# Performance work log

Hardware: AMD Instinct MI355X
Metric: run time of the kernel (lower is better)

## Reference

```python
import jax, jax.numpy as jnp
import numpy as np

NB_STEPS = 50
ALPHA = 0.9
NUM_RNN_STEPS = 2
B = 4096
NUM_FEATURE = 100
IN_D = 5
HIDDEN = [64, 64, 64]
P1 = (1.1, 1.1, 1.5, 2.0, 2.5)   # IntegrandNN_outer_level powers
P2 = (1.5, 2.0, 2.5, 3.0, 3.5)   # IntegrandNN powers


def _cc(nb_steps):
    # Clenshaw-Curtis weights/steps, identical to UMNN's compute_cc_weights
    n = nb_steps
    i = np.arange(n + 1, dtype=np.float64).reshape(-1, 1)
    lam = np.cos(i @ i.T * np.pi / n)
    lam[:, 0] = 0.5
    lam[:, -1] *= 0.5
    lam = lam * 2.0 / n
    W = np.zeros(n + 1)
    even = np.arange(0, n + 1, 2)
    W[even] = 2.0 / (1.0 - even.astype(np.float64) ** 2)
    W[0] = 1.0
    ccw = (lam.T @ W).astype(np.float32)                         # [n+1]
    steps = np.cos(np.arange(n + 1) * np.pi / n).astype(np.float32)  # [n+1]
    return jnp.asarray(ccw), jnp.asarray(steps)

CC_W, CC_S = _cc(NB_STEPS)


def _mlp(xh, Ws, bs):
    # Linear+ReLU stack with ELU on the last layer (ReLU popped, ELU appended)
    h = xh
    for W, b in zip(Ws[:-1], bs[:-1]):
        h = jax.nn.relu(h @ W.T + b)
    return jax.nn.elu(h @ Ws[-1].T + bs[-1])


def _integrand(x, h, Ws, bs, Wf, powers):
    z = _mlp(jnp.concatenate([x, h], axis=1), Ws, bs) + 1.0      # [N,1], z >= 0
    feats = jnp.concatenate([z ** p for p in powers], axis=1)    # [N,5]
    return jax.nn.relu((1.0 / (feats + 1.0)) @ Wf.T)             # [N,1]


def _integrate(x0, xT, h, f):
    # ParallelNeuralIntegral forward: CC quadrature of f from x0 to xT
    Bn, S = x0.shape[0], NB_STEPS + 1
    X = x0[:, None, :] + (xT - x0)[:, None, :] * (CC_S[None, :, None] + 1.0) / 2.0  # [B,S,1]
    hs = jnp.broadcast_to(h[:, None, :], (Bn, S, h.shape[1])).reshape(-1, h.shape[1])
    dz = f(X.reshape(-1, 1), hs).reshape(Bn, S, 1)
    return (dz * CC_W[None, :, None]).sum(1) * (xT - x0) / 2.0   # [B,1]


def setup_inputs() -> dict:
    key = jax.random.key(0)
    ks = jax.random.split(key, 24)
    def lin(k, o, i):
        return jax.random.normal(k, (o, i), jnp.float32) / np.sqrt(i)
    d = {}
    d["x_"] = jax.random.normal(ks[0], (B, NUM_FEATURE), jnp.float32)
    d["h_"] = jax.random.normal(ks[1], (B, IN_D - 1), jnp.float32)
    d["log_weight"] = jnp.ones((1, NUM_FEATURE), jnp.float32)     # reset_parameters -> 1
    d["sigmoid_param"] = jnp.zeros((1,), jnp.float32)
    sizes = [IN_D] + HIDDEN + [1]
    for tag, base in (("f1", 2), ("f2", 12)):
        for li, (i, o) in enumerate(zip(sizes[:-1], sizes[1:])):
            d[f"{tag}_W{li}"] = lin(ks[base + 2 * li], o, i)
            d[f"{tag}_b{li}"] = jnp.zeros((o,), jnp.float32)
        d[f"{tag}_Wf"] = jnp.abs(lin(ks[base + 9], 1, 5))         # reset_params -> abs
    return d


def reference(x_, h_, log_weight, sigmoid_param,
              f1_W0, f1_b0, f1_W1, f1_b1, f1_W2, f1_b2, f1_W3, f1_b3, f1_Wf,
              f2_W0, f2_b0, f2_W1, f2_b1, f2_W2, f2_b2, f2_W3, f2_b3, f2_Wf):
    f1Ws = [f1_W0, f1_W1, f1_W2, f1_W3]; f1bs = [f1_b0, f1_b1, f1_b2, f1_b3]
    f2Ws = [f2_W0, f2_W1, f2_W2, f2_W3]; f2bs = [f2_b0, f2_b1, f2_b2, f2_b3]
    f1 = lambda x, h: _integrand(x, h, f1Ws, f1bs, f1_Wf, P1)
    f2 = lambda x, h: _integrand(x, h, f2Ws, f2bs, f2_Wf, P2)

    # modular function: linear to [B,1] then sum over dim 1 -> [B,1]
    xm = jnp.sum(x_ * log_weight[0], axis=1, keepdims=True)
    lam = jax.nn.sigmoid(sigmoid_param[0])

    I1 = jnp.zeros_like(xm)
    I2 = jnp.zeros_like(xm)
    out_first = None
    for _ in range(NUM_RNN_STEPS):
        x = (1.0 - lam) * xm + lam * I1
        x2 = (1.0 - lam) * xm + lam * I2
        out_first = f1(x2, h_)
        I1 = _integrate(jnp.zeros_like(x), x, h_, f1)
        xmax = jnp.max(x2) + 10.0
        xfinal = jnp.zeros_like(x) + xmax
        I2 = (1.0 / ALPHA) * _integrate(x2, xfinal, h_, f2)
    return I1, out_first, I2
```

## Files before the change

### kernel.cpp

```cpp
#include <hip/hip_runtime.h>
#include <math.h>

typedef _Float16 half8v __attribute__((ext_vector_type(8)));
typedef _Float16 half4v __attribute__((ext_vector_type(4)));
typedef _Float16 half2v __attribute__((ext_vector_type(2)));
typedef float float4v __attribute__((ext_vector_type(4)));

#define BB    4096
#define INV_ALPHA (1.0f/0.9f)

#define WS_CCW  0
#define WS_CCS  64
#define WS_LAM  128
#define WS_PM16 160
#define WS_PM   256
#define WS_XM   512
#define WS_X    (WS_XM + BB)
#define WS_X2   (WS_X + BB)
#define WS_H    16384
#define H_NET   8192
#define H_W2    4096
#define H_W0    16384
#define H_W3    20480

#if defined(__has_builtin)
#if __has_builtin(__builtin_amdgcn_rcpf)
#define FRCP(x) __builtin_amdgcn_rcpf(x)
#endif
#if __has_builtin(__builtin_amdgcn_exp2f)
#define FEXP2(x) __builtin_amdgcn_exp2f(x)
#endif
#if __has_builtin(__builtin_amdgcn_logf)
#define FLOG2(x) __builtin_amdgcn_logf(x)
#endif
#endif
#ifndef FRCP
#define FRCP(x) (1.0f / (x))
#endif
#ifndef FEXP2
#define FEXP2(x) exp2f(x)
#endif
#ifndef FLOG2
#define FLOG2(x) log2f(x)
#endif

__device__ __forceinline__ int swz(int row, int cb) {
    return (row << 6) + (((cb ^ (row & 7)) & 7) << 3);
}

__device__ __forceinline__ half4v pk_relu4(float4v c) {
#if defined(__has_builtin) && __has_builtin(__builtin_amdgcn_cvt_pkrtz)
    half2v a = __builtin_bit_cast(half2v,
        __builtin_amdgcn_cvt_pkrtz(fmaxf(c[0], 0.0f), fmaxf(c[1], 0.0f)));
    half2v b = __builtin_bit_cast(half2v,
        __builtin_amdgcn_cvt_pkrtz(fmaxf(c[2], 0.0f), fmaxf(c[3], 0.0f)));
    half4v o; o[0] = a[0]; o[1] = a[1]; o[2] = b[0]; o[3] = b[1];
    return o;
#else
    half4v o;
    o[0] = (_Float16)fmaxf(c[0], 0.0f); o[1] = (_Float16)fmaxf(c[1], 0.0f);
    o[2] = (_Float16)fmaxf(c[2], 0.0f); o[3] = (_Float16)fmaxf(c[3], 0.0f);
    return o;
#endif
}

__global__ void k_setup(const float* __restrict__ x_, const float* __restrict__ lw,
                        const float* __restrict__ sp,
                        const float* __restrict__ f1W0, const float* __restrict__ f1W1,
                        const float* __restrict__ f1W2, const float* __restrict__ f1W3,
                        const float* __restrict__ f2W0, const float* __restrict__ f2W1,
                        const float* __restrict__ f2W2, const float* __restrict__ f2W3,
                        float* __restrict__ ws, float* __restrict__ out) {
    _Float16* wh = (_Float16*)(ws + WS_H);
    const int blk = blockIdx.x, tid = threadIdx.x;
    if (blk < 256) {
        int wave = tid >> 6, lane = tid & 63;
        float vmax = -1e30f;
        for (int r = 0; r < 4; ++r) {
            int row = blk * 16 + wave * 4 + r;
            float v = 0.0f;
            for (int i = lane; i < 100; i += 64) v = fmaf(x_[row * 100 + i], lw[i], v);
            #pragma unroll
            for (int off = 32; off > 0; off >>= 1) v += __shfl_xor(v, off, 64);
            if (lane == 0) ws[WS_XM + row] = v;
            vmax = fmaxf(vmax, v);
        }
        __shared__ float sm[4];
        if (lane == 0) sm[wave] = vmax;
        __syncthreads();
        if (tid == 0)
            ws[WS_PM + blk] = fmaxf(fmaxf(sm[0], sm[1]), fmaxf(sm[2], sm[3]));
    } else if (blk < 272) {
        int t = (blk - 256) * 256 + tid;
        wh[t]                = (_Float16)f1W1[t];
        wh[H_W2 + t]         = (_Float16)f1W2[t];
        wh[H_NET + t]        = (_Float16)f2W1[t];
        wh[H_NET + H_W2 + t] = (_Float16)f2W2[t];
        if (t < 2048) {
            int j = t >> 5, k = t & 31;
            wh[H_W0 + t]        = (k < 5) ? (_Float16)f1W0[j * 5 + k] : (_Float16)0.0f;
            wh[H_W0 + 2048 + t] = (k < 5) ? (_Float16)f2W0[j * 5 + k] : (_Float16)0.0f;
        }
        if (t < 64) {
            wh[H_W3 + t]      = (_Float16)f1W3[t];
            wh[H_W3 + 64 + t] = (_Float16)f2W3[t];
        }
    } else if (blk == 272) {
        if (tid == 64) ws[WS_LAM] = 1.0f / (1.0f + expf(-sp[0]));
        if (tid <= 50) {
            int s = tid;
            ws[WS_CCS + s] = cospif((float)s / 50.0f);
            float acc = 0.0f;
            for (int a = 0; a <= 50; ++a) {
                float w;
                if (a == 0) w = 1.0f;
                else if ((a & 1) == 0) w = 2.0f / (1.0f - (float)(a * a));
                else continue;
                float l;
                if (s == 0) l = 0.5f;
                else {
                    int m = (a * s) % 100;
                    l = cospif((float)m / 50.0f);
                    if (s == 50) l *= 0.5f;
                }
                acc += l * 0.04f * w;
            }
            ws[WS_CCW + s] = acc;
        }
    } else {
        int t = (blk - 273) * 256 + tid;
        out[t < BB ? t : BB + t] = 0.0f;
    }
}

__global__ void k_pre(float* __restrict__ ws, float* __restrict__ out) {
    int b = blockIdx.x * 256 + threadIdx.x;
    float lam = ws[WS_LAM];
    float m = ws[WS_XM + b];
    float xv  = (1.0f - lam) * m + lam * out[b];
    float x2v = (1.0f - lam) * m + lam * out[2 * BB + b];
    ws[WS_X + b] = xv;
    ws[WS_X2 + b] = x2v;
    out[b] = 0.0f;
    out[2 * BB + b] = 0.0f;
    __shared__ float red[256];
    red[threadIdx.x] = x2v;
    __syncthreads();
    #pragma unroll
    for (int off = 128; off > 0; off >>= 1) {
        if (threadIdx.x < off)
            red[threadIdx.x] = fmaxf(red[threadIdx.x], red[threadIdx.x + off]);
        __syncthreads();
    }
    if (threadIdx.x == 0) ws[WS_PM16 + blockIdx.x] = red[0];
}

__global__ __launch_bounds__(64, 2) void k_int(
    int mode, float* __restrict__ ws, const float* __restrict__ h_,
    const float* __restrict__ f1b0, const float* __restrict__ f1b1,
    const float* __restrict__ f1b2, const float* __restrict__ f1b3,
    const float* __restrict__ f1Wf,
    const float* __restrict__ f2b0, const float* __restrict__ f2b1,
    const float* __restrict__ f2b2, const float* __restrict__ f2b3,
    const float* __restrict__ f2Wf,
    float* __restrict__ out)
{
    __shared__ _Float16 act[64 * 64];

    const int blk = blockIdx.x;
    const int lane = threadIdx.x;
    const int lo = lane & 15, q = lane >> 4;

    const float* xm = ws + WS_XM;
    const float* xarr = ws + WS_X;
    const float* x2arr = ws + WS_X2;
    const _Float16* wh = (const _Float16*)(ws + WS_H);
    const float lam = ws[WS_LAM];
    const float oml = 1.0f - lam;

    const bool is_of = (blk >= 2048);
    int base, w = 0, np;
    bool u2;
    if (is_of) {
        base = (blk - 2048) << 6; u2 = false; np = 1;
    } else {
        int g = blk >> 4;
        w = blk & 15;
        u2 = (g >= 64);
        base = (g & 63) << 6;
        np = (w < 3) ? 4 : 3;
    }

    const _Float16* W0h = wh + H_W0 + (u2 ? 2048 : 0);
    const _Float16* W1h = wh + (u2 ? H_NET : 0);
    const _Float16* W2h = W1h + H_W2;
    const _Float16* W3h = wh + H_W3 + (u2 ? 64 : 0);
    const float* B0 = u2 ? f2b0 : f1b0;
    const float* B1 = u2 ? f2b1 : f1b1;
    const float* B2 = u2 ? f2b2 : f1b2;
    const float* B3 = u2 ? f2b3 : f1b3;
    const float* WF = u2 ? f2Wf : f1Wf;
    const float p0 = u2 ? 1.5f : 1.1f;
    const float p1 = u2 ? 2.0f : 1.1f;
    const float p2 = u2 ? 2.5f : 1.5f;
    const float p3 = u2 ? 3.0f : 2.0f;
    const float p4 = u2 ? 3.5f : 2.5f;

    half8v A0w[4], A1w[4][2], A2w[4][2];
    float4v b0r[4], b1r[4], b2r[4];
    half4v w3r[4];
    #pragma unroll
    for (int m = 0; m < 4; ++m) {
        A0w[m]    = *(const half8v*)(W0h + (16 * m + lo) * 32 + q * 8);
        A1w[m][0] = *(const half8v*)(W1h + (16 * m + lo) * 64 + q * 8);
        A1w[m][1] = *(const half8v*)(W1h + (16 * m + lo) * 64 + 32 + q * 8);
        A2w[m][0] = *(const half8v*)(W2h + (16 * m + lo) * 64 + q * 8);
        A2w[m][1] = *(const half8v*)(W2h + (16 * m + lo) * 64 + 32 + q * 8);
        b0r[m] = *(const float4v*)(B0 + 16 * m + q * 4);
        b1r[m] = *(const float4v*)(B1 + 16 * m + q * 4);
        b2r[m] = *(const float4v*)(B2 + 16 * m + q * 4);
        w3r[m] = *(const half4v*)(W3h + 16 * m + 4 * q);
    }
    const float B3s = B3[0];
    const float wf0 = WF[0], wf1 = WF[1], wf2 = WF[2], wf3 = WF[3], wf4 = WF[4];

    float xr_r[4];
    float4 h4r[4];
    #pragma unroll
    for (int n = 0; n < 4; ++n) {
        int idx = base + 16 * n + lo;
        float v;
        if (is_of)      v = x2arr[idx];
        else if (mode)  v = u2 ? x2arr[idx] : xarr[idx];
        else            v = oml * xm[idx];
        xr_r[n] = v;
        h4r[n] = ((const float4*)h_)[idx];
    }

    float xmax = 0.0f;
    if (u2) {
        if (mode) {
            float v = (lane < 16) ? ws[WS_PM16 + lane] : -1e30f;
            #pragma unroll
            for (int off = 32; off > 0; off >>= 1) v = fmaxf(v, __shfl_xor(v, off, 64));
            xmax = v + 10.0f;
        } else {
            const float* pm = ws + WS_PM;
            float v = fmaxf(fmaxf(pm[lane], pm[lane + 64]),
                            fmaxf(pm[lane + 128], pm[lane + 192]));
            #pragma unroll
            for (int off = 32; off > 0; off >>= 1) v = fmaxf(v, __shfl_xor(v, off, 64));
            xmax = oml * v + 10.0f;
        }
    }

    float acc = 0.0f;

    #pragma clang loop unroll(disable)
    for (int p = 0; p < np; ++p) {
        const int s = w + 16 * p;
        float t = 0.0f, ccw_s = 0.0f;
        if (!is_of) {
            t = (ws[WS_CCS + s] + 1.0f) * 0.5f;
            ccw_s = ws[WS_CCW + s];
        }

        half8v Bf0[4];
        #pragma unroll
        for (int n = 0; n < 4; ++n) {
            float xin;
            if (is_of)   xin = xr_r[n];
            else if (u2) xin = fmaf(t, xmax - xr_r[n], xr_r[n]);
            else         xin = xr_r[n] * t;
            half8v e;
            e[0] = (_Float16)xin; e[1] = (_Float16)h4r[n].x; e[2] = (_Float16)h4r[n].y;
            e[3] = (_Float16)h4r[n].z; e[4] = (_Float16)h4r[n].w;
            e[5] = (_Float16)0.0f; e[6] = (_Float16)0.0f; e[7] = (_Float16)0.0f;
            half8v z;
            #pragma unroll
            for (int t2 = 0; t2 < 8; ++t2) z[t2] = (_Float16)0.0f;
            Bf0[n] = (q == 0) ? e : z;
        }

        #pragma unroll
        for (int m = 0; m < 4; ++m)
            #pragma unroll
            for (int n = 0; n < 4; ++n) {
                float4v c = __builtin_amdgcn_mfma_f32_16x16x32_f16(A0w[m], Bf0[n], b0r[m], 0, 0, 0);
                *(half4v*)(act + swz(16 * n + lo, 2 * m + (q >> 1)) + 4 * (q & 1)) = pk_relu4(c);
            }

        {
            half8v Bf[2][4];
            #pragma unroll
            for (int kb = 0; kb < 2; ++kb)
                #pragma unroll
                for (int n = 0; n < 4; ++n)
                    Bf[kb][n] = *(const half8v*)(act + swz(16 * n + lo, 4 * kb + q));
            #pragma unroll
            for (int m = 0; m < 4; ++m)
                #pragma unroll
                for (int n = 0; n < 4; ++n) {
                    float4v c = __builtin_amdgcn_mfma_f32_16x16x32_f16(A1w[m][0], Bf[0][n], b1r[m], 0, 0, 0);
                    c = __builtin_amdgcn_mfma_f32_16x16x32_f16(A1w[m][1], Bf[1][n], c, 0, 0, 0);
                    *(half4v*)(act + swz(16 * n + lo, 2 * m + (q >> 1)) + 4 * (q & 1)) = pk_relu4(c);
                }
        }

        float part[4] = {0.0f, 0.0f, 0.0f, 0.0f};
        {
            half8v Bf[2][4];
            #pragma unroll
            for (int kb = 0; kb < 2; ++kb)
                #pragma unroll
                for (int n = 0; n < 4; ++n)
                    Bf[kb][n] = *(const half8v*)(act + swz(16 * n + lo, 4 * kb + q));
            #pragma unroll
            for (int m = 0; m < 4; ++m)
                #pragma unroll
                for (int n = 0; n < 4; ++n) {
                    float4v c = __builtin_amdgcn_mfma_f32_16x16x32_f16(A2w[m][0], Bf[0][n], b2r[m], 0, 0, 0);
                    c = __builtin_amdgcn_mfma_f32_16x16x32_f16(A2w[m][1], Bf[1][n], c, 0, 0, 0);
                    #pragma unroll
                    for (int e = 0; e < 4; ++e)
                        part[n] = fmaf((float)w3r[m][e], fmaxf(c[e], 0.0f), part[n]);
                }
        }

        #pragma unroll
        for (int n = 0; n < 4; ++n) {
            part[n] += __shfl_xor(part[n], 16, 64);
            part[n] += __shfl_xor(part[n], 32, 64);
        }
        float y = B3s + (q == 0 ? part[0] : q == 1 ? part[1] : q == 2 ? part[2] : part[3]);

        if (y <= 0.0f) y = FEXP2(y * 1.44269504f) - 1.0f;
        float z = y + 1.0f;
        float lg = FLOG2(z);
        float g = wf0 * FRCP(FEXP2(p0 * lg) + 1.0f)
                + wf1 * FRCP(FEXP2(p1 * lg) + 1.0f)
                + wf2 * FRCP(FEXP2(p2 * lg) + 1.0f)
                + wf3 * FRCP(FEXP2(p3 * lg) + 1.0f)
                + wf4 * FRCP(FEXP2(p4 * lg) + 1.0f);
        float val = fmaxf(g, 0.0f);

        if (is_of) { out[BB + base + lane] = val; return; }
        acc += ccw_s * val;
    }

    const float x_l = (q == 0 ? xr_r[0] : q == 1 ? xr_r[1] : q == 2 ? xr_r[2] : xr_r[3]);
    if (!u2) {
        atomicAdd(out + base + lane, acc * x_l * 0.5f);
    } else {
        atomicAdd(out + 2 * BB + base + lane, acc * (xmax - x_l) * 0.5f * INV_ALPHA);
    }
}

extern "C" void kernel_launch(void* const* d_in, const int* in_sizes, int n_in,
                              void* d_out, int out_size, void* d_ws, size_t ws_size,
                              hipStream_t stream) {
    const float* x_  = (const float*)d_in[0];
    const float* h_  = (const float*)d_in[1];
    const float* lw  = (const float*)d_in[2];
    const float* sp  = (const float*)d_in[3];
    const float* f1W0 = (const float*)d_in[4];   const float* f1b0 = (const float*)d_in[5];
    const float* f1W1 = (const float*)d_in[6];   const float* f1b1 = (const float*)d_in[7];
    const float* f1W2 = (const float*)d_in[8];   const float* f1b2 = (const float*)d_in[9];
    const float* f1W3 = (const float*)d_in[10];  const float* f1b3 = (const float*)d_in[11];
    const float* f1Wf = (const float*)d_in[12];
    const float* f2W0 = (const float*)d_in[13];  const float* f2b0 = (const float*)d_in[14];
    const float* f2W1 = (const float*)d_in[15];  const float* f2b1 = (const float*)d_in[16];
    const float* f2W2 = (const float*)d_in[17];  const float* f2b2 = (const float*)d_in[18];
    const float* f2W3 = (const float*)d_in[19];  const float* f2b3 = (const float*)d_in[20];
    const float* f2Wf = (const float*)d_in[21];
    float* out = (float*)d_out;
    float* ws  = (float*)d_ws;

    k_setup<<<305, 256, 0, stream>>>(x_, lw, sp,
                                     f1W0, f1W1, f1W2, f1W3,
                                     f2W0, f2W1, f2W2, f2W3, ws, out);
    k_int<<<2048, 64, 0, stream>>>(0, ws, h_,
        f1b0, f1b1, f1b2, f1b3, f1Wf, f2b0, f2b1, f2b2, f2b3, f2Wf, out);
    k_pre<<<16, 256, 0, stream>>>(ws, out);
    k_int<<<2112, 64, 0, stream>>>(1, ws, h_,
        f1b0, f1b1, f1b2, f1b3, f1Wf, f2b0, f2b1, f2b2, f2b3, f2Wf, out);
}
```

Measured before the change: 144.4 us.

## Split quadrature steps across more blocks and load weights per layer

Doubles the k_int grid so each 64-thread block handles 1-2 quadrature steps instead of 3-4, raising parallelism. MLP weight fragments are now loaded from global/L2 inside each layer loop rather than kept in registers for the whole kernel, and launch bounds go to 3 waves per EU to raise occupancy. k_pre switches to 64-thread blocks with a wavefront shuffle reduction, so xmax reads exactly 64 partial maxima. The cost is redundant weight and bias loads per block and more atomics or partial-sum writes.

After: 225.7 us. +56.3%, slower.

```diff
diff --git a/kernel.cpp b/kernel.cpp
--- a/kernel.cpp
+++ b/kernel.cpp
@@ -134,7 +134,7 @@
 }
 
 __global__ void k_pre(float* __restrict__ ws, float* __restrict__ out) {
-    int b = blockIdx.x * 256 + threadIdx.x;
+    int b = blockIdx.x * 64 + threadIdx.x;
     float lam = ws[WS_LAM];
     float m = ws[WS_XM + b];
     float xv  = (1.0f - lam) * m + lam * out[b];
@@ -143,19 +143,13 @@
     ws[WS_X2 + b] = x2v;
     out[b] = 0.0f;
     out[2 * BB + b] = 0.0f;
-    __shared__ float red[256];
-    red[threadIdx.x] = x2v;
-    __syncthreads();
+    float v = x2v;
     #pragma unroll
-    for (int off = 128; off > 0; off >>= 1) {
-        if (threadIdx.x < off)
-            red[threadIdx.x] = fmaxf(red[threadIdx.x], red[threadIdx.x + off]);
-        __syncthreads();
-    }
-    if (threadIdx.x == 0) ws[WS_PM16 + blockIdx.x] = red[0];
-}
-
-__global__ __launch_bounds__(64, 2) void k_int(
+    for (int off = 32; off > 0; off >>= 1) v = fmaxf(v, __shfl_xor(v, off, 64));
+    if (threadIdx.x == 0) ws[WS_PM16 + blockIdx.x] = v;
+}
+
+__global__ __launch_bounds__(64, 3) void k_int(
     int mode, float* __restrict__ ws, const float* __restrict__ h_,
     const float* __restrict__ f1b0, const float* __restrict__ f1b1,
     const float* __restrict__ f1b2, const float* __restrict__ f1b3,
@@ -178,17 +172,17 @@
     const float lam = ws[WS_LAM];
     const float oml = 1.0f - lam;
 
-    const bool is_of = (blk >= 2048);
+    const bool is_of = (blk >= 4096);
     int base, w = 0, np;
     bool u2;
     if (is_of) {
-        base = (blk - 2048) << 6; u2 = false; np = 1;
+        base = (blk - 4096) << 6; u2 = false; np = 1;
     } else {
-        int g = blk >> 4;
-        w = blk & 15;
+        int g = blk >> 5;
+        w = blk & 31;
         u2 = (g >= 64);
         base = (g & 63) << 6;
-        np = (w < 3) ? 4 : 3;
+        np = (w <= 18) ? 2 : 1;
     }
 
     const _Float16* W0h = wh + H_W0 + (u2 ? 2048 : 0);
@@ -206,16 +200,10 @@
     const float p3 = u2 ? 3.0f : 2.0f;
     const float p4 = u2 ? 3.5f : 2.5f;
 
-    half8v A0w[4], A1w[4][2], A2w[4][2];
     float4v b0r[4], b1r[4], b2r[4];
     half4v w3r[4];
     #pragma unroll
     for (int m = 0; m < 4; ++m) {
-        A0w[m]    = *(const half8v*)(W0h + (16 * m + lo) * 32 + q * 8);
-        A1w[m][0] = *(const half8v*)(W1h + (16 * m + lo) * 64 + q * 8);
-        A1w[m][1] = *(const half8v*)(W1h + (16 * m + lo) * 64 + 32 + q * 8);
-        A2w[m][0] = *(const half8v*)(W2h + (16 * m + lo) * 64 + q * 8);
-        A2w[m][1] = *(const half8v*)(W2h + (16 * m + lo) * 64 + 32 + q * 8);
         b0r[m] = *(const float4v*)(B0 + 16 * m + q * 4);
         b1r[m] = *(const float4v*)(B1 + 16 * m + q * 4);
         b2r[m] = *(const float4v*)(B2 + 16 * m + q * 4);
@@ -240,7 +228,7 @@
     float xmax = 0.0f;
     if (u2) {
         if (mode) {
-            float v = (lane < 16) ? ws[WS_PM16 + lane] : -1e30f;
+            float v = ws[WS_PM16 + lane];
             #pragma unroll
             for (int off = 32; off > 0; off >>= 1) v = fmaxf(v, __shfl_xor(v, off, 64));
             xmax = v + 10.0f;
@@ -258,7 +246,7 @@
 
     #pragma clang loop unroll(disable)
     for (int p = 0; p < np; ++p) {
-        const int s = w + 16 * p;
+        const int s = w + 32 * p;
         float t = 0.0f, ccw_s = 0.0f;
         if (!is_of) {
             t = (ws[WS_CCS + s] + 1.0f) * 0.5f;
@@ -283,12 +271,14 @@
         }
 
         #pragma unroll
-        for (int m = 0; m < 4; ++m)
+        for (int m = 0; m < 4; ++m) {
+            half8v a0 = *(const half8v*)(W0h + (16 * m + lo) * 32 + q * 8);
             #pragma unroll
             for (int n = 0; n < 4; ++n) {
-                float4v c = __builtin_amdgcn_mfma_f32_16x16x32_f16(A0w[m], Bf0[n], b0r[m], 0, 0, 0);
+                float4v c = __builtin_amdgcn_mfma_f32_16x16x32_f16(a0, Bf0[n], b0r[m], 0, 0, 0);
                 *(half4v*)(act + swz(16 * n + lo, 2 * m + (q >> 1)) + 4 * (q & 1)) = pk_relu4(c);
             }
+        }
 
         {
             half8v Bf[2][4];
@@ -298,13 +288,16 @@
                 for (int n = 0; n < 4; ++n)
                     Bf[kb][n] = *(const half8v*)(act + swz(16 * n + lo, 4 * kb + q));
             #pragma unroll
-            for (int m = 0; m < 4; ++m)
+            for (int m = 0; m < 4; ++m) {
+                half8v a10 = *(const half8v*)(W1h + (16 * m + lo) * 64 + q * 8);
+                half8v a11 = *(const half8v*)(W1h + (16 * m + lo) * 64 + 32 + q * 8);
                 #pragma unroll
                 for (int n = 0; n < 4; ++n) {
-                    float4v c = __builtin_amdgcn_mfma_f32_16x16x32_f16(A1w[m][0], Bf[0][n], b1r[m], 0, 0, 0);
-                    c = __builtin_amdgcn_mfma_f32_16x16x32_f16(A1w[m][1], Bf[1][n], c, 0, 0, 0);
+                    float4v c = __builtin_amdgcn_mfma_f32_16x16x32_f16(a10, Bf[0][n], b1r[m], 0, 0, 0);
+                    c = __builtin_amdgcn_mfma_f32_16x16x32_f16(a11, Bf[1][n], c, 0, 0, 0);
                     *(half4v*)(act + swz(16 * n + lo, 2 * m + (q >> 1)) + 4 * (q & 1)) = pk_relu4(c);
                 }
+            }
         }
 
         float part[4] = {0.0f, 0.0f, 0.0f, 0.0f};
@@ -316,15 +309,18 @@
                 for (int n = 0; n < 4; ++n)
                     Bf[kb][n] = *(const half8v*)(act + swz(16 * n + lo, 4 * kb + q));
             #pragma unroll
-            for (int m = 0; m < 4; ++m)
+            for (int m = 0; m < 4; ++m) {
+                half8v a20 = *(const half8v*)(W2h + (16 * m + lo) * 64 + q * 8);
+                half8v a21 = *(const half8v*)(W2h + (16 * m + lo) * 64 + 32 + q * 8);
                 #pragma unroll
                 for (int n = 0; n < 4; ++n) {
-                    float4v c = __builtin_amdgcn_mfma_f32_16x16x32_f16(A2w[m][0], Bf[0][n], b2r[m], 0, 0, 0);
-                    c = __builtin_amdgcn_mfma_f32_16x16x32_f16(A2w[m][1], Bf[1][n], c, 0, 0, 0);
+                    float4v c = __builtin_amdgcn_mfma_f32_16x16x32_f16(a20, Bf[0][n], b2r[m], 0, 0, 0);
+                    c = __builtin_amdgcn_mfma_f32_16x16x32_f16(a21, Bf[1][n], c, 0, 0, 0);
                     #pragma unroll
                     for (int e = 0; e < 4; ++e)
                         part[n] = fmaf((float)w3r[m][e], fmaxf(c[e], 0.0f), part[n]);
                 }
+            }
         }
 
         #pragma unroll
@@ -379,9 +375,9 @@
     k_setup<<<305, 256, 0, stream>>>(x_, lw, sp,
                                      f1W0, f1W1, f1W2, f1W3,
                                      f2W0, f2W1, f2W2, f2W3, ws, out);
-    k_int<<<2048, 64, 0, stream>>>(0, ws, h_,
+    k_int<<<4096, 64, 0, stream>>>(0, ws, h_,
         f1b0, f1b1, f1b2, f1b3, f1Wf, f2b0, f2b1, f2b2, f2b3, f2Wf, out);
-    k_pre<<<16, 256, 0, stream>>>(ws, out);
-    k_int<<<2112, 64, 0, stream>>>(1, ws, h_,
+    k_pre<<<64, 64, 0, stream>>>(ws, out);
+    k_int<<<4160, 64, 0, stream>>>(1, ws, h_,
         f1b0, f1b1, f1b2, f1b3, f1Wf, f2b0, f2b1, f2b2, f2b3, f2Wf, out);
 }
```

## Evaluate two quadrature nodes per iteration and fold out_first into idle slots

Applied to the files above, without the earlier changes.

The integrand loop now runs two quadrature nodes per iteration, interleaving two independent MLP evaluations through a doubled LDS activation buffer. This gives the MFMA and transcendental sequences more independent work to overlap. The bias vectors move from registers into shared memory to make room for the larger live state. The out_first evaluation, previously done by 64 extra blocks, now uses the otherwise idle second slot of the w==15 waves, so the second launch shrinks to 2048 blocks. The costs are more register pressure, which risks spills, and some wasted padded evaluations for waves with only three nodes.

Result: slower. 169.0 us (+17.1%).

```diff
diff --git a/kernel.cpp b/kernel.cpp
--- a/kernel.cpp
+++ b/kernel.cpp
@@ -62,6 +62,20 @@
     o[2] = (_Float16)fmaxf(c[2], 0.0f); o[3] = (_Float16)fmaxf(c[3], 0.0f);
     return o;
 #endif
+}
+
+__device__ __forceinline__ float tail5(float y,
+        float p0, float p1, float p2, float p3, float p4,
+        float wf0, float wf1, float wf2, float wf3, float wf4) {
+    if (y <= 0.0f) y = FEXP2(y * 1.44269504f) - 1.0f;
+    float z = y + 1.0f;
+    float lg = FLOG2(z);
+    float g = wf0 * FRCP(FEXP2(p0 * lg) + 1.0f)
+            + wf1 * FRCP(FEXP2(p1 * lg) + 1.0f)
+            + wf2 * FRCP(FEXP2(p2 * lg) + 1.0f)
+            + wf3 * FRCP(FEXP2(p3 * lg) + 1.0f)
+            + wf4 * FRCP(FEXP2(p4 * lg) + 1.0f);
+    return fmaxf(g, 0.0f);
 }
 
 __global__ void k_setup(const float* __restrict__ x_, const float* __restrict__ lw,
@@ -165,7 +179,8 @@
     const float* __restrict__ f2Wf,
     float* __restrict__ out)
 {
-    __shared__ _Float16 act[64 * 64];
+    __shared__ _Float16 act[2 * 64 * 64];
+    __shared__ float bl[192];
 
     const int blk = blockIdx.x;
     const int lane = threadIdx.x;
@@ -178,18 +193,11 @@
     const float lam = ws[WS_LAM];
     const float oml = 1.0f - lam;
 
-    const bool is_of = (blk >= 2048);
-    int base, w = 0, np;
-    bool u2;
-    if (is_of) {
-        base = (blk - 2048) << 6; u2 = false; np = 1;
-    } else {
-        int g = blk >> 4;
-        w = blk & 15;
-        u2 = (g >= 64);
-        base = (g & 63) << 6;
-        np = (w < 3) ? 4 : 3;
-    }
+    const int g = blk >> 4;
+    const int w = blk & 15;
+    const bool u2 = (g >= 64);
+    const int base = (g & 63) << 6;
+    const bool of_wave = (mode != 0) && (!u2) && (w == 15);
 
     const _Float16* W0h = wh + H_W0 + (u2 ? 2048 : 0);
     const _Float16* W1h = wh + (u2 ? H_NET : 0);
@@ -206,8 +214,11 @@
     const float p3 = u2 ? 3.0f : 2.0f;
     const float p4 = u2 ? 3.5f : 2.5f;
 
+    bl[lane]       = B0[lane];
+    bl[64 + lane]  = B1[lane];
+    bl[128 + lane] = B2[lane];
+
     half8v A0w[4], A1w[4][2], A2w[4][2];
-    float4v b0r[4], b1r[4], b2r[4];
     half4v w3r[4];
     #pragma unroll
     for (int m = 0; m < 4; ++m) {
@@ -216,25 +227,23 @@
         A1w[m][1] = *(const half8v*)(W1h + (16 * m + lo) * 64 + 32 + q * 8);
         A2w[m][0] = *(const half8v*)(W2h + (16 * m + lo) * 64 + q * 8);
         A2w[m][1] = *(const half8v*)(W2h + (16 * m + lo) * 64 + 32 + q * 8);
-        b0r[m] = *(const float4v*)(B0 + 16 * m + q * 4);
-        b1r[m] = *(const float4v*)(B1 + 16 * m + q * 4);
-        b2r[m] = *(const float4v*)(B2 + 16 * m + q * 4);
         w3r[m] = *(const half4v*)(W3h + 16 * m + 4 * q);
     }
     const float B3s = B3[0];
     const float wf0 = WF[0], wf1 = WF[1], wf2 = WF[2], wf3 = WF[3], wf4 = WF[4];
 
-    float xr_r[4];
+    float xr_r[4], x2_r[4];
     float4 h4r[4];
     #pragma unroll
     for (int n = 0; n < 4; ++n) {
         int idx = base + 16 * n + lo;
-        float v;
-        if (is_of)      v = x2arr[idx];
-        else if (mode)  v = u2 ? x2arr[idx] : xarr[idx];
-        else            v = oml * xm[idx];
-        xr_r[n] = v;
+        xr_r[n] = mode ? (u2 ? x2arr[idx] : xarr[idx]) : oml * xm[idx];
         h4r[n] = ((const float4*)h_)[idx];
+        x2_r[n] = 0.0f;
+    }
+    if (of_wave) {
+        #pragma unroll
+        for (int n = 0; n < 4; ++n) x2_r[n] = x2arr[base + 16 * n + lo];
     }
 
     float xmax = 0.0f;
@@ -257,95 +266,114 @@
     float acc = 0.0f;
 
     #pragma clang loop unroll(disable)
-    for (int p = 0; p < np; ++p) {
-        const int s = w + 16 * p;
-        float t = 0.0f, ccw_s = 0.0f;
-        if (!is_of) {
-            t = (ws[WS_CCS + s] + 1.0f) * 0.5f;
-            ccw_s = ws[WS_CCW + s];
-        }
-
-        half8v Bf0[4];
+    for (int dp = 0; dp < 2; ++dp) {
+        const int s0 = w + 32 * dp;
+        const bool live1 = (dp == 0) || (w < 3);
+        const int s1 = live1 ? (s0 + 16) : s0;
+        const bool of1 = of_wave && (dp == 1);
+        const float t0 = (ws[WS_CCS + s0] + 1.0f) * 0.5f;
+        const float cw0 = ws[WS_CCW + s0];
+        const float t1 = (ws[WS_CCS + s1] + 1.0f) * 0.5f;
+        const float cw1 = live1 ? ws[WS_CCW + s1] : 0.0f;
+
+        half8v Bf0[2][4];
         #pragma unroll
-        for (int n = 0; n < 4; ++n) {
-            float xin;
-            if (is_of)   xin = xr_r[n];
-            else if (u2) xin = fmaf(t, xmax - xr_r[n], xr_r[n]);
-            else         xin = xr_r[n] * t;
-            half8v e;
-            e[0] = (_Float16)xin; e[1] = (_Float16)h4r[n].x; e[2] = (_Float16)h4r[n].y;
-            e[3] = (_Float16)h4r[n].z; e[4] = (_Float16)h4r[n].w;
-            e[5] = (_Float16)0.0f; e[6] = (_Float16)0.0f; e[7] = (_Float16)0.0f;
-            half8v z;
-            #pragma unroll
-            for (int t2 = 0; t2 < 8; ++t2) z[t2] = (_Float16)0.0f;
-            Bf0[n] = (q == 0) ? e : z;
+        for (int j = 0; j < 2; ++j) {
+            const float tj = j ? t1 : t0;
+            #pragma unroll
+            for (int n = 0; n < 4; ++n) {
+                float xin;
+                if (j == 1 && of1) xin = x2_r[n];
+                else if (u2)       xin = fmaf(tj, xmax - xr_r[n], xr_r[n]);
+                else               xin = xr_r[n] * tj;
+                half8v e;
+                e[0] = (_Float16)xin; e[1] = (_Float16)h4r[n].x; e[2] = (_Float16)h4r[n].y;
+                e[3] = (_Float16)h4r[n].z; e[4] = (_Float16)h4r[n].w;
+                e[5] = (_Float16)0.0f; e[6] = (_Float16)0.0f; e[7] = (_Float16)0.0f;
+                half8v z;
+                #pragma unroll
+                for (int t2 = 0; t2 < 8; ++t2) z[t2] = (_Float16)0.0f;
+                Bf0[j][n] = (q == 0) ? e : z;
+            }
         }
 
         #pragma unroll
-        for (int m = 0; m < 4; ++m)
+        for (int m = 0; m < 4; ++m) {
+            float4v b0 = *(const float4v*)(bl + 16 * m + 4 * q);
+            #pragma unroll
+            for (int j = 0; j < 2; ++j)
+                #pragma unroll
+                for (int n = 0; n < 4; ++n) {
+                    float4v c = __builtin_amdgcn_mfma_f32_16x16x32_f16(A0w[m], Bf0[j][n], b0, 0, 0, 0);
+                    *(half4v*)(act + j * 4096 + swz(16 * n + lo, 2 * m + (q >> 1)) + 4 * (q & 1)) = pk_relu4(c);
+                }
+        }
+
+        {
+            half8v Bf[2][2][4];
+            #pragma unroll
+            for (int j = 0; j < 2; ++j)
+                #pragma unroll
+                for (int kb = 0; kb < 2; ++kb)
+                    #pragma unroll
+                    for (int n = 0; n < 4; ++n)
+                        Bf[j][kb][n] = *(const half8v*)(act + j * 4096 + swz(16 * n + lo, 4 * kb + q));
+            #pragma unroll
+            for (int m = 0; m < 4; ++m) {
+                float4v b1 = *(const float4v*)(bl + 64 + 16 * m + 4 * q);
+                #pragma unroll
+                for (int j = 0; j < 2; ++j)
+                    #pragma unroll
+                    for (int n = 0; n < 4; ++n) {
+                        float4v c = __builtin_amdgcn_mfma_f32_16x16x32_f16(A1w[m][0], Bf[j][0][n], b1, 0, 0, 0);
+                        c = __builtin_amdgcn_mfma_f32_16x16x32_f16(A1w[m][1], Bf[j][1][n], c, 0, 0, 0);
+                        *(half4v*)(act + j * 4096 + swz(16 * n + lo, 2 * m + (q >> 1)) + 4 * (q & 1)) = pk_relu4(c);
+                    }
+            }
+        }
+
+        float part[2][4] = {{0.0f, 0.0f, 0.0f, 0.0f}, {0.0f, 0.0f, 0.0f, 0.0f}};
+        {
+            half8v Bf[2][2][4];
+            #pragma unroll
+            for (int j = 0; j < 2; ++j)
+                #pragma unroll
+                for (int kb = 0; kb < 2; ++kb)
+                    #pragma unroll
+                    for (int n = 0; n < 4; ++n)
+                        Bf[j][kb][n] = *(const half8v*)(act + j * 4096 + swz(16 * n + lo, 4 * kb + q));
+            #pragma unroll
+            for (int m = 0; m < 4; ++m) {
+                float4v b2 = *(const float4v*)(bl + 128 + 16 * m + 4 * q);
+                #pragma unroll
+                for (int j = 0; j < 2; ++j)
+                    #pragma unroll
+                    for (int n = 0; n < 4; ++n) {
+                        float4v c = __builtin_amdgcn_mfma_f32_16x16x32_f16(A2w[m][0], Bf[j][0][n], b2, 0, 0, 0);
+                        c = __builtin_amdgcn_mfma_f32_16x16x32_f16(A2w[m][1], Bf[j][1][n], c, 0, 0, 0);
+                        #pragma unroll
+                        for (int e = 0; e < 4; ++e)
+                            part[j][n] = fmaf((float)w3r[m][e], fmaxf(c[e], 0.0f), part[j][n]);
+                    }
+            }
+        }
+
+        #pragma unroll
+        for (int j = 0; j < 2; ++j)
             #pragma unroll
             for (int n = 0; n < 4; ++n) {
-                float4v c = __builtin_amdgcn_mfma_f32_16x16x32_f16(A0w[m], Bf0[n], b0r[m], 0, 0, 0);
-                *(half4v*)(act + swz(16 * n + lo, 2 * m + (q >> 1)) + 4 * (q & 1)) = pk_relu4(c);
+                part[j][n] += __shfl_xor(part[j][n], 16, 64);
+                part[j][n] += __shfl_xor(part[j][n], 32, 64);
             }
-
-        {
-            half8v Bf[2][4];
-            #pragma unroll
-            for (int kb = 0; kb < 2; ++kb)
-                #pragma unroll
-                for (int n = 0; n < 4; ++n)
-                    Bf[kb][n] = *(const half8v*)(act + swz(16 * n + lo, 4 * kb + q));
-            #pragma unroll
-            for (int m = 0; m < 4; ++m)
-                #pragma unroll
-                for (int n = 0; n < 4; ++n) {
-                    float4v c = __builtin_amdgcn_mfma_f32_16x16x32_f16(A1w[m][0], Bf[0][n], b1r[m], 0, 0, 0);
-                    c = __builtin_amdgcn_mfma_f32_16x16x32_f16(A1w[m][1], Bf[1][n], c, 0, 0, 0);
-                    *(half4v*)(act + swz(16 * n + lo, 2 * m + (q >> 1)) + 4 * (q & 1)) = pk_relu4(c);
-                }
-        }
-
-        float part[4] = {0.0f, 0.0f, 0.0f, 0.0f};
-        {
-            half8v Bf[2][4];
-            #pragma unroll
-            for (int kb = 0; kb < 2; ++kb)
-                #pragma unroll
-                for (int n = 0; n < 4; ++n)
-                    Bf[kb][n] = *(const half8v*)(act + swz(16 * n + lo, 4 * kb + q));
-            #pragma unroll
-            for (int m = 0; m < 4; ++m)
-                #pragma unroll
-                for (int n = 0; n < 4; ++n) {
-                    float4v c = __builtin_amdgcn_mfma_f32_16x16x32_f16(A2w[m][0], Bf[0][n], b2r[m], 0, 0, 0);
-                    c = __builtin_amdgcn_mfma_f32_16x16x32_f16(A2w[m][1], Bf[1][n], c, 0, 0, 0);
-                    #pragma unroll
-                    for (int e = 0; e < 4; ++e)
-                        part[n] = fmaf((float)w3r[m][e], fmaxf(c[e], 0.0f), part[n]);
-                }
-        }
-
-        #pragma unroll
-        for (int n = 0; n < 4; ++n) {
-            part[n] += __shfl_xor(part[n], 16, 64);
-            part[n] += __shfl_xor(part[n], 32, 64);
-        }
-        float y = B3s + (q == 0 ? part[0] : q == 1 ? part[1] : q == 2 ? part[2] : part[3]);
-
-        if (y <= 0.0f) y = FEXP2(y * 1.44269504f) - 1.0f;
-        float z = y + 1.0f;
-        float lg = FLOG2(z);
-        float g = wf0 * FRCP(FEXP2(p0 * lg) + 1.0f)
-                + wf1 * FRCP(FEXP2(p1 * lg) + 1.0f)
-                + wf2 * FRCP(FEXP2(p2 * lg) + 1.0f)
-                + wf3 * FRCP(FEXP2(p3 * lg) + 1.0f)
-                + wf4 * FRCP(FEXP2(p4 * lg) + 1.0f);
-        float val = fmaxf(g, 0.0f);
-
-        if (is_of) { out[BB + base + lane] = val; return; }
-        acc += ccw_s * val;
+        float y0 = B3s + (q == 0 ? part[0][0] : q == 1 ? part[0][1] : q == 2 ? part[0][2] : part[0][3]);
+        float y1 = B3s + (q == 0 ? part[1][0] : q == 1 ? part[1][1] : q == 2 ? part[1][2] : part[1][3]);
+
+        float val0 = tail5(y0, p0, p1, p2, p3, p4, wf0, wf1, wf2, wf3, wf4);
+        float val1 = tail5(y1, p0, p1, p2, p3, p4, wf0, wf1, wf2, wf3, wf4);
+
+        acc = fmaf(cw0, val0, acc);
+        acc = fmaf(cw1, val1, acc);
+        if (of1) out[BB + base + lane] = val1;
     }
 
     const float x_l = (q == 0 ? xr_r[0] : q == 1 ? xr_r[1] : q == 2 ? xr_r[2] : xr_r[3]);
@@ -382,6 +410,6 @@
     k_int<<<2048, 64, 0, stream>>>(0, ws, h_,
         f1b0, f1b1, f1b2, f1b3, f1Wf, f2b0, f2b1, f2b2, f2b3, f2Wf, out);
     k_pre<<<16, 256, 0, stream>>>(ws, out);
-    k_int<<<2112, 64, 0, stream>>>(1, ws, h_,
+    k_int<<<2048, 64, 0, stream>>>(1, ws, h_,
         f1b0, f1b1, f1b2, f1b3, f1Wf, f2b0, f2b1, f2b2, f2b3, f2Wf, out);
 }
```
